# Kernel optimization log

Hardware: AMD Instinct MI355X
Metric: run time of the kernel (lower is better)

Reference implementation:

```python
import jax, jax.numpy as jnp
import numpy as np

H = 300          # node_hidden_dim (GINE output dim)
D = 2 * H        # set2set in_channels = 600
STEPS = 2        # num_step_set2_set


def _lstm_cell(x, h, c, W_ih, W_hh, b_ih, b_hh):
    # PyTorch LSTM gate order: i, f, g, o
    gates = x @ W_ih.T + h @ W_hh.T + b_ih + b_hh
    i, f, g, o = jnp.split(gates, 4, axis=-1)
    c = jax.nn.sigmoid(f) * c + jax.nn.sigmoid(i) * jnp.tanh(g)
    h = jax.nn.sigmoid(o) * jnp.tanh(c)
    return h, c


def _set2set(x, batch, num_graphs, W_ih, W_hh, b_ih, b_hh):
    # torch_geometric Set2Set with processing_steps=STEPS, 1-layer LSTM
    B = num_graphs
    q_star = jnp.zeros((B, 2 * D), x.dtype)
    h = jnp.zeros((B, D), x.dtype)
    c = jnp.zeros((B, D), x.dtype)
    for _ in range(STEPS):
        h, c = _lstm_cell(q_star, h, c, W_ih, W_hh, b_ih, b_hh)
        q = h                                   # [B, D]
        e = jnp.sum(x * q[batch], axis=-1)      # [N]
        emax = jax.ops.segment_max(e, batch, num_segments=B)
        a = jnp.exp(e - emax[batch])
        asum = jax.ops.segment_sum(a, batch, num_segments=B)
        a = a / (asum[batch] + 1e-16)           # segment softmax
        r = jax.ops.segment_sum(a[:, None] * x, batch, num_segments=B)
        q_star = jnp.concatenate([q, r], axis=-1)   # [B, 2D]
    return q_star


def _l2norm(x):
    return x / jnp.maximum(jnp.linalg.norm(x, axis=1, keepdims=True), 1e-12)


def setup_inputs() -> dict:
    key = jax.random.key(0)
    ks = jax.random.split(key, 8)
    Nu, Nv, B = 8192, 8192, 256
    solute_x = jax.random.normal(ks[0], (Nu, H), jnp.float32)
    solvent_x = jax.random.normal(ks[1], (Nv, H), jnp.float32)
    solute_batch = jnp.sort(jax.random.randint(ks[2], (Nu,), 0, B)).astype(jnp.int32)
    solvent_batch = jnp.sort(jax.random.randint(ks[3], (Nv,), 0, B)).astype(jnp.int32)
    lstm_W_ih = jax.random.normal(ks[4], (4 * D, 2 * D), jnp.float32) * 0.02
    lstm_W_hh = jax.random.normal(ks[5], (4 * D, D), jnp.float32) * 0.02
    lstm_b_ih = jnp.zeros((4 * D,), jnp.float32)
    lstm_b_hh = jnp.zeros((4 * D,), jnp.float32)
    pred_W = jax.random.normal(ks[6], (1, 8 * H), jnp.float32) * 0.02
    pred_b = jnp.zeros((1,), jnp.float32)
    return {
        "solute_x": solute_x, "solvent_x": solvent_x,
        "solute_batch": solute_batch, "solvent_batch": solvent_batch,
        "num_graphs": B,
        "lstm_W_ih": lstm_W_ih, "lstm_W_hh": lstm_W_hh,
        "lstm_b_ih": lstm_b_ih, "lstm_b_hh": lstm_b_hh,
        "pred_W": pred_W, "pred_b": pred_b,
    }


def reference(solute_x, solvent_x, solute_batch, solvent_batch, num_graphs,
              lstm_W_ih, lstm_W_hh, lstm_b_ih, lstm_b_hh, pred_W, pred_b):
    # F.normalize(dim=1)
    su = _l2norm(solute_x)    # [Nu, H]
    sv = _l2norm(solvent_x)   # [Nv, H]
    # len_map = solute_len.T @ solvent_len == same-pair membership mask
    mask = (solute_batch[:, None] == solvent_batch[None, :]).astype(su.dtype)
    interaction_map = (su @ sv.T) * mask          # [Nu, Nv]
    ret_interaction_map = interaction_map
    solvent_prime = interaction_map.T @ su        # [Nv, H]
    solute_prime = interaction_map @ sv           # [Nu, H]
    su2 = jnp.concatenate([su, solute_prime], axis=1)    # [Nu, 2H]
    sv2 = jnp.concatenate([sv, solvent_prime], axis=1)   # [Nv, 2H]
    su_s2s = _set2set(su2, solute_batch, num_graphs, lstm_W_ih, lstm_W_hh, lstm_b_ih, lstm_b_hh)
    sv_s2s = _set2set(sv2, solvent_batch, num_graphs, lstm_W_ih, lstm_W_hh, lstm_b_ih, lstm_b_hh)
    final = jnp.concatenate([su_s2s, sv_s2s], axis=1)    # [B, 8H]
    predictions = final @ pred_W.T + pred_b              # [B, 1]
    return predictions, ret_interaction_map
```

## Files before the change

kernel.cpp:

```cpp
#include <hip/hip_runtime.h>
#include <math.h>

#define HDIM 300
#define DDIM 600
#define NGR  256

typedef float vf4 __attribute__((ext_vector_type(4)));

__device__ __forceinline__ float wred_sum(float v){
  #pragma unroll
  for(int o=32;o;o>>=1) v += __shfl_xor(v,o,64);
  return v;
}
__device__ __forceinline__ float wred_max(float v){
  #pragma unroll
  for(int o=32;o;o>>=1) v = fmaxf(v,__shfl_xor(v,o,64));
  return v;
}
__device__ __forceinline__ float sigm(float x){ return 1.f/(1.f+expf(-x)); }

__global__ __launch_bounds__(256) void k_norm_off(const float* __restrict__ xu,
    const float* __restrict__ xv, float* __restrict__ su, float* __restrict__ sv,
    int Nu, int Nv, const int* __restrict__ ub, const int* __restrict__ vb,
    int* __restrict__ uoff, int* __restrict__ voff,
    const float* __restrict__ b_ih, const float* __restrict__ b_hh,
    float* __restrict__ h1, float* __restrict__ c1,
    const float* __restrict__ pb, float* __restrict__ outp){
  if (blockIdx.x == gridDim.x - 1){
    int t = threadIdx.x;
    if (t < NGR){
      int lo=0, hi=Nu;
      while(lo<hi){ int m=(lo+hi)>>1; if (ub[m] < t) lo=m+1; else hi=m; }
      uoff[t]=lo;
      lo=0; hi=Nv;
      while(lo<hi){ int m=(lo+hi)>>1; if (vb[m] < t) lo=m+1; else hi=m; }
      voff[t]=lo;
      if (t==0){ uoff[NGR]=Nu; voff[NGR]=Nv; }
      outp[t] = pb[0];
    }
    for (int d=threadIdx.x; d<DDIM; d+=256){
      float gi = b_ih[d]      + b_hh[d];
      float gg = b_ih[1200+d] + b_hh[1200+d];
      float go = b_ih[1800+d] + b_hh[1800+d];
      float c  = sigm(gi)*tanhf(gg);
      c1[d]=c; h1[d]=sigm(go)*tanhf(c);
    }
    return;
  }
  int wid = blockIdx.x*4 + (threadIdx.x >> 6);
  int lane = threadIdx.x & 63;
  const float* src; float* dst;
  if (wid < Nu){ src = xu + (size_t)wid*HDIM; dst = su + (size_t)wid*HDIM; }
  else         { src = xv + (size_t)(wid-Nu)*HDIM; dst = sv + (size_t)(wid-Nu)*HDIM; }
  const vf4* s4 = (const vf4*)src;
  vf4 A = s4[lane];
  vf4 Bv = (lane<11)? s4[64+lane] : (vf4){0.f,0.f,0.f,0.f};
  float s = A.x*A.x+A.y*A.y+A.z*A.z+A.w*A.w + Bv.x*Bv.x+Bv.y*Bv.y+Bv.z*Bv.z+Bv.w*Bv.w;
  s = wred_sum(s);
  float inv = 1.f / fmaxf(sqrtf(s), 1e-12f);
  vf4* d4 = (vf4*)dst;
  d4[lane] = A*inv;
  if (lane<11) d4[64+lane] = Bv*inv;
}

__global__ __launch_bounds__(256) void k_prime(const float* __restrict__ su,
    const float* __restrict__ sv, const int* __restrict__ ub,
    const int* __restrict__ vb, const int* __restrict__ uoff,
    const int* __restrict__ voff, float* __restrict__ spr,
    float* __restrict__ svp, float* __restrict__ e1u, float* __restrict__ e1v,
    const float* __restrict__ h1, float* __restrict__ mapbase, int Nu, int Nv){
  int b = blockIdx.x;
  bool isU = (b < Nu);
  int i = isU ? b : b - Nu;
  const float* xa = isU ? su : sv;
  const float* xb = isU ? sv : su;
  const int* mybatch = isU ? ub : vb;
  const int* ooff    = isU ? voff : uoff;
  float* prime = isU ? spr : svp;
  float* eout  = isU ? e1u : e1v;

  int tid = threadIdx.x, lane = tid & 63, w = tid >> 6;
  __shared__ __align__(16) float xrow[304];
  __shared__ __align__(16) float prl[4*304];
  __shared__ float qv[2*HDIM];
  __shared__ float red[4];
  const float* rowp = xa + (size_t)i*HDIM;
  for (int t=tid; t<HDIM;   t+=256) xrow[t] = rowp[t];
  for (int t=tid; t<2*HDIM; t+=256) qv[t]   = h1[t];
  int g = mybatch[i];
  int js = ooff[g], je = ooff[g+1];
  __syncthreads();

  if (isU){
    float* mrow = mapbase + (size_t)i*Nv;
    const vf4 z4 = {0.f,0.f,0.f,0.f};
    int nf4 = Nv >> 2;
    for (int q4=tid; q4<nf4; q4+=256){
      int j0 = q4*4;
      if (j0+4 <= js || j0 >= je){
        __builtin_nontemporal_store(z4, (vf4*)(mrow + j0));
      } else {
        #pragma unroll
        for(int u=0;u<4;u++){ int j=j0+u; if (j<js || j>=je) mrow[j]=0.f; }
      }
    }
  }

  const vf4* x4 = (const vf4*)xrow;
  vf4 xA = x4[lane];
  vf4 xB = (lane<11)? x4[64+lane] : (vf4){0.f,0.f,0.f,0.f};
  vf4 prA = {0.f,0.f,0.f,0.f}, prB = {0.f,0.f,0.f,0.f};
  for (int j = js + w; j < je; j += 4){
    const vf4* orow = (const vf4*)(xb + (size_t)j*HDIM);
    vf4 oA = orow[lane];
    vf4 oB = (lane<11)? orow[64+lane] : (vf4){0.f,0.f,0.f,0.f};
    float d = oA.x*xA.x + oA.y*xA.y + oA.z*xA.z + oA.w*xA.w
            + oB.x*xB.x + oB.y*xB.y + oB.z*xB.z + oB.w*xB.w;
    d = wred_sum(d);
    if (isU && lane==0) mapbase[(size_t)i*Nv + j] = d;
    prA += d * oA;
    prB += d * oB;
  }
  vf4* p4 = (vf4*)(prl + w*304);
  p4[lane] = prA;
  if (lane<11) p4[64+lane] = prB;
  __syncthreads();
  float ep = 0.f;
  for (int t=tid; t<HDIM; t+=256){
    float s = prl[t] + prl[304+t] + prl[608+t] + prl[912+t];
    prime[(size_t)i*HDIM + t] = s;
    ep += xrow[t]*qv[t] + s*qv[HDIM+t];
  }
  ep = wred_sum(ep);
  if (lane==0) red[w] = ep;
  __syncthreads();
  if (tid==0) eout[i] = red[0]+red[1]+red[2]+red[3];
}

__global__ __launch_bounds__(256) void k_r1_gbase(const float* __restrict__ su,
    const float* __restrict__ sv, const float* __restrict__ spr,
    const float* __restrict__ svp, const float* __restrict__ e1u,
    const float* __restrict__ e1v, const int* __restrict__ uoff,
    const int* __restrict__ voff, float* __restrict__ r1,
    const float* __restrict__ h1, const float* __restrict__ Wih,
    const float* __restrict__ Whh, const float* __restrict__ b_ih,
    const float* __restrict__ b_hh, float* __restrict__ gbase){
  int tid = threadIdx.x, lane = tid & 63, w = tid >> 6;
  if (blockIdx.x >= 512){
    int n = (blockIdx.x - 512)*4 + w;
    if (n >= 2400) return;
    const float* wi = Wih + (size_t)n*1200;
    const float* wh = Whh + (size_t)n*600;
    float s = 0.f;
    for (int k=lane; k<DDIM; k+=64) s += h1[k]*(wi[k] + wh[k]);
    s = wred_sum(s);
    if (lane==0) gbase[n] = s + b_ih[n] + b_hh[n];
    return;
  }
  int bs = blockIdx.x; int set = bs >> 8; int g = bs & 255;
  const float* x  = set? sv  : su;
  const float* pr = set? svp : spr;
  const float* e  = set? e1v : e1u;
  const int* off  = set? voff: uoff;
  __shared__ float al[2048]; __shared__ float red[4]; __shared__ float shv;
  int ns = off[g], ne = off[g+1]; int n = ne - ns;
  float m = -INFINITY;
  for (int t=ns+tid; t<ne; t+=256) m = fmaxf(m, e[t]);
  m = wred_max(m);
  if (lane==0) red[w]=m;
  __syncthreads();
  if (tid==0) shv = fmaxf(fmaxf(red[0],red[1]),fmaxf(red[2],red[3]));
  __syncthreads();
  float emax = shv;
  float s = 0.f;
  for (int t=tid; t<n; t+=256){ float a = expf(e[ns+t]-emax); if (t<2048) al[t]=a; s += a; }
  s = wred_sum(s);
  __syncthreads();
  if (lane==0) red[w]=s;
  __syncthreads();
  if (tid==0) shv = red[0]+red[1]+red[2]+red[3];
  __syncthreads();
  float inv = 1.f/(shv + 1e-16f);
  float acc[3] = {0.f,0.f,0.f};
  for (int nn=0; nn<n; nn++){
    float a = (nn<2048)? al[nn] : expf(e[ns+nn]-emax);
    const float* xr = x  + (size_t)(ns+nn)*HDIM;
    const float* pp = pr + (size_t)(ns+nn)*HDIM;
    #pragma unroll
    for(int u=0;u<3;u++){ int c = tid + u*256; if (c<DDIM){
        float xv = (c<HDIM)? xr[c] : pp[c-HDIM]; acc[u] += a*xv; } }
  }
  #pragma unroll
  for(int u=0;u<3;u++){ int c = tid + u*256; if (c<DDIM) r1[(size_t)bs*DDIM + c] = acc[u]*inv; }
}

__global__ __launch_bounds__(256) void k_gemm_lstm(const float* __restrict__ r1,
    const float* __restrict__ Wih, const float* __restrict__ gbase,
    const float* __restrict__ c1, float* __restrict__ h2){
  __shared__ __align__(16) float smem[64*68];
  float* Al = smem;
  float* Bl = smem + 16*68;
  int tid = threadIdx.x;
  int d0  = blockIdx.x*16;
  int gs0 = blockIdx.y*64;
  int tx = tid & 15, ty = tid >> 4;
  int lk = tid & 15, lr = tid >> 4;
  float acc[4][4] = {};
  for (int kt=0; kt<600; kt+=16){
    int k = kt + lk;
    bool kok = (k < 600);
    #pragma unroll
    for (int u=0; u<4; u++){
      int rl = lr + u*16;
      Al[lk*68 + rl] = kok ? r1[(size_t)(gs0+rl)*DDIM + k] : 0.f;
      int gate = rl >> 4, dd = rl & 15;
      int d = d0 + dd;
      Bl[lk*68 + rl] = (kok && d < 600)
          ? Wih[(size_t)(gate*600 + d)*1200 + 600 + k] : 0.f;
    }
    __syncthreads();
    #pragma unroll
    for (int kk=0; kk<16; kk++){
      vf4 av = ((const vf4*)(Al + kk*68))[ty];
      vf4 bv = ((const vf4*)(Bl + kk*68))[tx];
      float a[4]={av.x,av.y,av.z,av.w}, bb[4]={bv.x,bv.y,bv.z,bv.w};
      #pragma unroll
      for(int mm=0;mm<4;mm++)
        #pragma unroll
        for(int nn=0;nn<4;nn++) acc[mm][nn] += a[mm]*bb[nn];
    }
    __syncthreads();
  }
  #pragma unroll
  for (int mm=0; mm<4; mm++){
    vf4 o = {acc[mm][0], acc[mm][1], acc[mm][2], acc[mm][3]};
    ((vf4*)(smem + (ty*4+mm)*68))[tx] = o;
  }
  __syncthreads();
  int d_l = tid & 15, r0 = tid >> 4;
  int d = d0 + d_l;
  if (d < 600){
    float gb_i = gbase[d], gb_f = gbase[600+d], gb_g = gbase[1200+d], gb_o = gbase[1800+d];
    float cc1 = c1[d];
    #pragma unroll
    for (int u=0; u<4; u++){
      int rl = r0 + u*16;
      const float* gr = smem + rl*68;
      float gi = gr[d_l]      + gb_i;
      float gf = gr[16+d_l]   + gb_f;
      float gG = gr[32+d_l]   + gb_g;
      float go = gr[48+d_l]   + gb_o;
      float c  = sigm(gf)*cc1 + sigm(gi)*tanhf(gG);
      h2[(size_t)(gs0+rl)*DDIM + d] = sigm(go)*tanhf(c);
    }
  }
}

__global__ __launch_bounds__(256) void k_r2(const float* __restrict__ su,
    const float* __restrict__ sv, const float* __restrict__ spr,
    const float* __restrict__ svp, const int* __restrict__ uoff,
    const int* __restrict__ voff, const float* __restrict__ h2,
    const float* __restrict__ pW, float* __restrict__ e2u,
    float* __restrict__ e2v, float* __restrict__ outp){
  int bs = blockIdx.x; int set = bs >> 8; int g = bs & 255;
  const float* x  = set? sv  : su;
  const float* pr = set? svp : spr;
  const int* off  = set? voff: uoff;
  float* e2       = set? e2v : e2u;
  int tid = threadIdx.x, lane = tid & 63, w = tid >> 6;
  __shared__ float q[DDIM]; __shared__ float al[2048];
  __shared__ float red[4]; __shared__ float shv;
  for (int t=tid; t<DDIM; t+=256) q[t] = h2[(size_t)bs*DDIM + t];
  int ns = off[g], ne = off[g+1]; int n = ne - ns;
  __syncthreads();
  for (int node = ns + w; node < ne; node += 4){
    const float* xr = x  + (size_t)node*HDIM;
    const float* pp = pr + (size_t)node*HDIM;
    float d = 0.f;
    #pragma unroll
    for(int c=0;c<10;c++){ int k = lane + 64*c; if (k<DDIM){
        float xv = (k<HDIM)? xr[k] : pp[k-HDIM]; d += xv*q[k]; } }
    d = wred_sum(d);
    if (lane==0) e2[node] = d;
  }
  __syncthreads();
  float m = -INFINITY;
  for (int t=ns+tid; t<ne; t+=256) m = fmaxf(m, e2[t]);
  m = wred_max(m);
  if (lane==0) red[w]=m;
  __syncthreads();
  if (tid==0) shv = fmaxf(fmaxf(red[0],red[1]),fmaxf(red[2],red[3]));
  __syncthreads();
  float emax = shv;
  float s = 0.f;
  for (int t=tid; t<n; t+=256){ float a = expf(e2[ns+t]-emax); if (t<2048) al[t]=a; s += a; }
  s = wred_sum(s);
  __syncthreads();
  if (lane==0) red[w]=s;
  __syncthreads();
  if (tid==0) shv = red[0]+red[1]+red[2]+red[3];
  __syncthreads();
  float inv = 1.f/(shv + 1e-16f);
  float acc[3] = {0.f,0.f,0.f};
  for (int nn=0; nn<n; nn++){
    float a = (nn<2048)? al[nn] : expf(e2[ns+nn]-emax);
    const float* xr = x  + (size_t)(ns+nn)*HDIM;
    const float* pp = pr + (size_t)(ns+nn)*HDIM;
    #pragma unroll
    for(int u=0;u<3;u++){ int c = tid + u*256; if (c<DDIM){
        float xv = (c<HDIM)? xr[c] : pp[c-HDIM]; acc[u] += a*xv; } }
  }
  int hoff = set? 1200 : 0;
  float p = 0.f;
  #pragma unroll
  for(int u=0;u<3;u++){ int c = tid + u*256; if (c<DDIM) p += (acc[u]*inv)*pW[hoff+600+c]; }
  for (int t=tid; t<DDIM; t+=256) p += q[t]*pW[hoff+t];
  p = wred_sum(p);
  __syncthreads();
  if (lane==0) red[w] = p;
  __syncthreads();
  if (tid==0) atomicAdd(&outp[g], red[0]+red[1]+red[2]+red[3]);
}

extern "C" void kernel_launch(void* const* d_in, const int* in_sizes, int n_in,
                              void* d_out, int out_size, void* d_ws, size_t ws_size,
                              hipStream_t stream) {
  const float* solute_x  = (const float*)d_in[0];
  const float* solvent_x = (const float*)d_in[1];
  const int*   ub        = (const int*)d_in[2];
  const int*   vb        = (const int*)d_in[3];
  const float* Wih  = (const float*)d_in[5];
  const float* Whh  = (const float*)d_in[6];
  const float* b_ih = (const float*)d_in[7];
  const float* b_hh = (const float*)d_in[8];
  const float* pW   = (const float*)d_in[9];
  const float* pb   = (const float*)d_in[10];

  int Nu = in_sizes[0] / HDIM;
  int Nv = in_sizes[1] / HDIM;

  float* out = (float*)d_out;
  int predn = out_size - Nu*Nv;
  float* mapbase = out + predn;

  float* ws = (float*)d_ws;
  float* su    = ws;
  float* sv    = su    + (size_t)Nu*HDIM;
  float* spr   = sv    + (size_t)Nv*HDIM;
  float* svp   = spr   + (size_t)Nu*HDIM;
  float* e1u   = svp   + (size_t)Nv*HDIM;
  float* e1v   = e1u   + Nu;
  float* h1    = e1v   + Nv;
  float* c1    = h1    + DDIM;
  float* r1    = c1    + DDIM;
  float* gbase = r1    + 512*DDIM;
  float* h2    = gbase + 2400;
  int*   uoff  = (int*)(h2 + 512*DDIM);
  int*   voff  = uoff + 257;

  k_norm_off<<<dim3((Nu+Nv)/4 + 1), dim3(256), 0, stream>>>(
      solute_x, solvent_x, su, sv, Nu, Nv, ub, vb, uoff, voff,
      b_ih, b_hh, h1, c1, pb, out);
  k_prime<<<dim3(Nu+Nv), dim3(256), 0, stream>>>(
      su, sv, ub, vb, uoff, voff, spr, svp, e1u, e1v, h1, mapbase, Nu, Nv);
  k_r1_gbase<<<dim3(512+600), dim3(256), 0, stream>>>(
      su, sv, spr, svp, e1u, e1v, uoff, voff, r1, h1, Wih, Whh, b_ih, b_hh, gbase);
  k_gemm_lstm<<<dim3(38, 8), dim3(256), 0, stream>>>(r1, Wih, gbase, c1, h2);
  k_r2<<<dim3(512), dim3(256), 0, stream>>>(
      su, sv, spr, svp, uoff, voff, h2, pW, e1u, e1v, out);
}
```

Measured before the change: 576.5 us.

## Move interaction-map zero fill into norm kernel and halve LSTM GEMM row tile

The masked zero fill of the large Nu×Nv interaction map moves out of k_prime into the first normalization kernel as Nu extra blocks. Each of those blocks binary-searches its solvent range itself, since the offsets are not ready yet. This takes the heavy store stream off the compute-bound prime kernel and lets it run alongside the normalization blocks. The LSTM gate GEMM also drops its row tile from 64 to 32, doubling the grid to fill more CUs, at the cost of reloading each W tile twice as often.

```diff
diff --git a/kernel.cpp b/kernel.cpp
--- a/kernel.cpp
+++ b/kernel.cpp
@@ -6,6 +6,7 @@
 #define NGR  256
 
 typedef float vf4 __attribute__((ext_vector_type(4)));
+typedef float vf2 __attribute__((ext_vector_type(2)));
 
 __device__ __forceinline__ float wred_sum(float v){
   #pragma unroll
@@ -19,14 +20,17 @@
 }
 __device__ __forceinline__ float sigm(float x){ return 1.f/(1.f+expf(-x)); }
 
-__global__ __launch_bounds__(256) void k_norm_off(const float* __restrict__ xu,
+__global__ __launch_bounds__(256) void k_norm_fill_off(const float* __restrict__ xu,
     const float* __restrict__ xv, float* __restrict__ su, float* __restrict__ sv,
     int Nu, int Nv, const int* __restrict__ ub, const int* __restrict__ vb,
     int* __restrict__ uoff, int* __restrict__ voff,
     const float* __restrict__ b_ih, const float* __restrict__ b_hh,
     float* __restrict__ h1, float* __restrict__ c1,
-    const float* __restrict__ pb, float* __restrict__ outp){
-  if (blockIdx.x == gridDim.x - 1){
+    const float* __restrict__ pb, float* __restrict__ outp,
+    float* __restrict__ mapbase){
+  int NBn = (Nu + Nv) >> 2;
+  int b = blockIdx.x;
+  if (b == NBn){
     int t = threadIdx.x;
     if (t < NGR){
       int lo=0, hi=Nu;
@@ -47,7 +51,30 @@
     }
     return;
   }
-  int wid = blockIdx.x*4 + (threadIdx.x >> 6);
+  if (b > NBn){
+    int i = b - NBn - 1;
+    int g = ub[i];
+    int lo=0, hi=Nv;
+    while(lo<hi){ int m=(lo+hi)>>1; if (vb[m] < g) lo=m+1; else hi=m; }
+    int js = lo;
+    hi = Nv;
+    while(lo<hi){ int m=(lo+hi)>>1; if (vb[m] <= g) lo=m+1; else hi=m; }
+    int je = lo;
+    float* mrow = mapbase + (size_t)i*Nv;
+    const vf4 z4 = {0.f,0.f,0.f,0.f};
+    int nf4 = Nv >> 2;
+    for (int q4=threadIdx.x; q4<nf4; q4+=256){
+      int j0 = q4*4;
+      if (j0+4 <= js || j0 >= je){
+        __builtin_nontemporal_store(z4, (vf4*)(mrow + j0));
+      } else {
+        #pragma unroll
+        for(int u=0;u<4;u++){ int j=j0+u; if (j<js || j>=je) mrow[j]=0.f; }
+      }
+    }
+    return;
+  }
+  int wid = b*4 + (threadIdx.x >> 6);
   int lane = threadIdx.x & 63;
   const float* src; float* dst;
   if (wid < Nu){ src = xu + (size_t)wid*HDIM; dst = su + (size_t)wid*HDIM; }
@@ -90,21 +117,6 @@
   int g = mybatch[i];
   int js = ooff[g], je = ooff[g+1];
   __syncthreads();
-
-  if (isU){
-    float* mrow = mapbase + (size_t)i*Nv;
-    const vf4 z4 = {0.f,0.f,0.f,0.f};
-    int nf4 = Nv >> 2;
-    for (int q4=tid; q4<nf4; q4+=256){
-      int j0 = q4*4;
-      if (j0+4 <= js || j0 >= je){
-        __builtin_nontemporal_store(z4, (vf4*)(mrow + j0));
-      } else {
-        #pragma unroll
-        for(int u=0;u<4;u++){ int j=j0+u; if (j<js || j>=je) mrow[j]=0.f; }
-      }
-    }
-  }
 
   const vf4* x4 = (const vf4*)xrow;
   vf4 xA = x4[lane];
@@ -197,44 +209,47 @@
 __global__ __launch_bounds__(256) void k_gemm_lstm(const float* __restrict__ r1,
     const float* __restrict__ Wih, const float* __restrict__ gbase,
     const float* __restrict__ c1, float* __restrict__ h2){
-  __shared__ __align__(16) float smem[64*68];
+  __shared__ __align__(16) float smem[32*68];
   float* Al = smem;
-  float* Bl = smem + 16*68;
+  float* Bl = smem + 16*36;
   int tid = threadIdx.x;
   int d0  = blockIdx.x*16;
-  int gs0 = blockIdx.y*64;
+  int gs0 = blockIdx.y*32;
   int tx = tid & 15, ty = tid >> 4;
-  int lk = tid & 15, lr = tid >> 4;
-  float acc[4][4] = {};
+  float acc[2][4] = {};
   for (int kt=0; kt<600; kt+=16){
-    int k = kt + lk;
+    int k = kt + tx;
     bool kok = (k < 600);
     #pragma unroll
+    for (int u=0; u<2; u++){
+      int rl = ty + u*16;
+      Al[tx*36 + rl] = kok ? r1[(size_t)(gs0+rl)*DDIM + k] : 0.f;
+    }
+    #pragma unroll
     for (int u=0; u<4; u++){
-      int rl = lr + u*16;
-      Al[lk*68 + rl] = kok ? r1[(size_t)(gs0+rl)*DDIM + k] : 0.f;
-      int gate = rl >> 4, dd = rl & 15;
+      int cl = ty + u*16;
+      int gate = cl >> 4, dd = cl & 15;
       int d = d0 + dd;
-      Bl[lk*68 + rl] = (kok && d < 600)
+      Bl[tx*68 + cl] = (kok && d < 600)
           ? Wih[(size_t)(gate*600 + d)*1200 + 600 + k] : 0.f;
     }
     __syncthreads();
     #pragma unroll
     for (int kk=0; kk<16; kk++){
-      vf4 av = ((const vf4*)(Al + kk*68))[ty];
+      vf2 av = ((const vf2*)(Al + kk*36))[ty];
       vf4 bv = ((const vf4*)(Bl + kk*68))[tx];
-      float a[4]={av.x,av.y,av.z,av.w}, bb[4]={bv.x,bv.y,bv.z,bv.w};
+      float a[2]={av.x,av.y}, bb[4]={bv.x,bv.y,bv.z,bv.w};
       #pragma unroll
-      for(int mm=0;mm<4;mm++)
+      for(int mm=0;mm<2;mm++)
         #pragma unroll
         for(int nn=0;nn<4;nn++) acc[mm][nn] += a[mm]*bb[nn];
     }
     __syncthreads();
   }
   #pragma unroll
-  for (int mm=0; mm<4; mm++){
+  for (int mm=0; mm<2; mm++){
     vf4 o = {acc[mm][0], acc[mm][1], acc[mm][2], acc[mm][3]};
-    ((vf4*)(smem + (ty*4+mm)*68))[tx] = o;
+    ((vf4*)(smem + (ty*2+mm)*68))[tx] = o;
   }
   __syncthreads();
   int d_l = tid & 15, r0 = tid >> 4;
@@ -243,7 +258,7 @@
     float gb_i = gbase[d], gb_f = gbase[600+d], gb_g = gbase[1200+d], gb_o = gbase[1800+d];
     float cc1 = c1[d];
     #pragma unroll
-    for (int u=0; u<4; u++){
+    for (int u=0; u<2; u++){
       int rl = r0 + u*16;
       const float* gr = smem + rl*68;
       float gi = gr[d_l]      + gb_i;
@@ -358,14 +373,15 @@
   int*   uoff  = (int*)(h2 + 512*DDIM);
   int*   voff  = uoff + 257;
 
-  k_norm_off<<<dim3((Nu+Nv)/4 + 1), dim3(256), 0, stream>>>(
+  int NBn = (Nu + Nv) / 4;
+  k_norm_fill_off<<<dim3(NBn + 1 + Nu), dim3(256), 0, stream>>>(
       solute_x, solvent_x, su, sv, Nu, Nv, ub, vb, uoff, voff,
-      b_ih, b_hh, h1, c1, pb, out);
+      b_ih, b_hh, h1, c1, pb, out, mapbase);
   k_prime<<<dim3(Nu+Nv), dim3(256), 0, stream>>>(
       su, sv, ub, vb, uoff, voff, spr, svp, e1u, e1v, h1, mapbase, Nu, Nv);
   k_r1_gbase<<<dim3(512+600), dim3(256), 0, stream>>>(
       su, sv, spr, svp, e1u, e1v, uoff, voff, r1, h1, Wih, Whh, b_ih, b_hh, gbase);
-  k_gemm_lstm<<<dim3(38, 8), dim3(256), 0, stream>>>(r1, Wih, gbase, c1, h2);
+  k_gemm_lstm<<<dim3(38, 16), dim3(256), 0, stream>>>(r1, Wih, gbase, c1, h2);
   k_r2<<<dim3(512), dim3(256), 0, stream>>>(
       su, sv, spr, svp, uoff, voff, h2, pW, e1u, e1v, out);
 }
```

After: 548.6 us. 4.8% less time.
